# Kernel optimization log

Measured on AMD Instinct MI355X. Metric: run time of the kernel, lower is better.

Reference implementation:

```python
import jax, jax.numpy as jnp
from jax import lax
import numpy as np

H, W = 240, 304
IN_CH, OUT_CH, K = 16, 32, 3
B = 8
N_PER = 65536
N = B * N_PER
CIN = IN_CH + 2  # pos + neg + features


def setup_inputs() -> dict:
    key = jax.random.key(0)
    k1, k2, k3, k4, k5 = jax.random.split(key, 5)
    # events columns: x, y, t in [0,1); polarity in {0,1}
    xyt = jax.random.uniform(k1, (N, 3), dtype=jnp.float32)
    pol = jax.random.randint(k2, (N, 1), 0, 2).astype(jnp.float32)
    events = jnp.concatenate([xyt, pol], axis=1)
    features = jax.random.normal(k3, (N, IN_CH), dtype=jnp.float32)
    offsets = (jnp.arange(1, B + 1, dtype=jnp.int64) * N_PER)  # cumulative counts
    # SubmanifoldConvolution params: one [CIN, OUT_CH] matrix per filter offset -> HWIO
    fan_in = K * K * CIN
    weight = jax.random.normal(k4, (K, K, CIN, OUT_CH), dtype=jnp.float32) / np.sqrt(fan_in)
    bias = jax.random.normal(k5, (OUT_CH,), dtype=jnp.float32) * 0.01
    return {"events": events, "features": features, "weight": weight,
            "bias": bias, "offsets": offsets}


def reference(events, features, weight, bias, offsets):
    n = events.shape[0]
    b = offsets.shape[0]
    # offset2batch: row i belongs to first sample whose cumulative offset exceeds i
    batch = jnp.searchsorted(offsets, jnp.arange(n, dtype=offsets.dtype), side="right").astype(jnp.int32)
    pos = events[:, 3:4]
    neg = 1.0 - pos
    sparse = jnp.concatenate([pos, neg, features], axis=1)  # [N, CIN]
    # yx = events[:, [1, 0]] scaled by (h, w), rounded to grid coords
    yi = jnp.clip(jnp.round(events[:, 1] * H).astype(jnp.int32), 0, H - 1)
    xi = jnp.clip(jnp.round(events[:, 0] * W).astype(jnp.int32), 0, W - 1)
    key = (batch * H + yi) * W + xi  # linear site id, [N]
    nseg = b * H * W
    # scn InputLayer mode=4: average features of duplicate coordinates
    feat_sum = jax.ops.segment_sum(sparse, key, num_segments=nseg)  # [nseg, CIN]
    cnt = jax.ops.segment_sum(jnp.ones((n,), sparse.dtype), key, num_segments=nseg)
    dense = feat_sum / jnp.maximum(cnt, 1.0)[:, None]
    dense = dense.reshape(b, H, W, CIN)  # zeros at inactive sites
    # Submanifold 3x3 conv: inactive neighbors are zero, so a dense SAME conv
    # evaluated only at active sites matches the submanifold rulebook math.
    out = lax.conv_general_dilated(dense, weight, window_strides=(1, 1),
                                   padding="SAME",
                                   dimension_numbers=("NHWC", "HWIO", "NHWC"))
    out = out.reshape(nseg, OUT_CH)
    # OutputLayer: read back per input row (active sites only), add bias there
    f = out[key] + bias  # [N, OUT_CH]
    return f
```

## Files before the change

kernel.cpp:

```cpp
#include <hip/hip_runtime.h>

#define Hh 240
#define Ww 304
#define IN_CH 16
#define OUT_CH 32
#define Bb 8
#define N_PER 65536
#define N_EV (Bb * N_PER)
#define CIN (IN_CH + 2)
#define NSEG (Bb * Hh * Ww)
#define NBLK 570

#define TW 32
#define TH 8
#define HW_ 34
#define HH_ 10
#define NXT_TILES 10
#define NYT_TILES 30
#define OPITCH 33

typedef __attribute__((ext_vector_type(8))) short bf16x8;
typedef __attribute__((ext_vector_type(4))) float f32x4;

__device__ __forceinline__ unsigned short f2bf(float x) {
  unsigned u = __float_as_uint(x);
  unsigned r = u + 0x7fffu + ((u >> 16) & 1u);
  return (unsigned short)(r >> 16);
}
__device__ __forceinline__ float bf2f(unsigned short b) {
  return __uint_as_float(((unsigned)b) << 16);
}

__global__ __launch_bounds__(256) void hist_rank_kernel(
    const float* __restrict__ events, const int* __restrict__ offsets,
    int* __restrict__ hist, int* __restrict__ keyArr, int* __restrict__ rankArr) {
  int i = blockIdx.x * blockDim.x + threadIdx.x;
  float4 ev = ((const float4*)events)[i];
  int yi = (int)rintf(ev.y * (float)Hh);
  yi = min(max(yi, 0), Hh - 1);
  int xi = (int)rintf(ev.x * (float)Ww);
  xi = min(max(xi, 0), Ww - 1);
  int b = 0;
#pragma unroll
  for (int j = 0; j < Bb; j++) b += (offsets[j] <= i) ? 1 : 0;
  int key = (b * Hh + yi) * Ww + xi;
  int pol = (ev.w != 0.0f) ? 1 : 0;
  keyArr[i] = key | (pol << 31);
  rankArr[i] = atomicAdd(&hist[key], 1);
}

__global__ __launch_bounds__(256) void scan1_kernel(
    const int* __restrict__ hist, int* __restrict__ baseLocal,
    int* __restrict__ blockSum) {
  __shared__ int lds[256];
  int b = blockIdx.x, t = threadIdx.x;
  int idx = b * 1024 + t * 4;
  int4 v = *(const int4*)(hist + idx);
  int s0 = v.x, s1 = s0 + v.y, s2 = s1 + v.z, s3 = s2 + v.w;
  lds[t] = s3;
  __syncthreads();
  int val = s3;
  for (int off = 1; off < 256; off <<= 1) {
    int n = (t >= off) ? lds[t - off] : 0;
    __syncthreads();
    val += n;
    lds[t] = val;
    __syncthreads();
  }
  int excl = val - s3;
  int4 o;
  o.x = excl; o.y = excl + s0; o.z = excl + s1; o.w = excl + s2;
  *(int4*)(baseLocal + idx) = o;
  if (t == 255) blockSum[b] = val;
}

__global__ __launch_bounds__(1024) void scan2_kernel(
    const int* __restrict__ blockSum, int* __restrict__ blockOffset) {
  __shared__ int lds[1024];
  int t = threadIdx.x;
  int v = (t < NBLK) ? blockSum[t] : 0;
  lds[t] = v;
  __syncthreads();
  int val = v;
  for (int off = 1; off < 1024; off <<= 1) {
    int n = (t >= off) ? lds[t - off] : 0;
    __syncthreads();
    val += n;
    lds[t] = val;
    __syncthreads();
  }
  if (t < NBLK) blockOffset[t] = val - v;
  if (t == 0) blockOffset[NBLK] = lds[1023];
}

__global__ __launch_bounds__(256) void scatter_feat_kernel(
    const float* __restrict__ features, const int* __restrict__ keyArr,
    const int* __restrict__ rankArr, const int* __restrict__ baseLocal,
    const int* __restrict__ blockOffset, uint4* __restrict__ sortedFeat,
    int* __restrict__ sortedMeta) {
  int i = blockIdx.x * blockDim.x + threadIdx.x;
  int meta = keyArr[i];
  int key = meta & 0x7fffffff;
  int pos = baseLocal[key] + blockOffset[key >> 10] + rankArr[i];
  const float4* f = (const float4*)(features + (size_t)i * IN_CH);
  float4 f0 = f[0], f1 = f[1], f2 = f[2], f3 = f[3];
  uint4 w0, w1;
  w0.x = (unsigned)f2bf(f0.x) | ((unsigned)f2bf(f0.y) << 16);
  w0.y = (unsigned)f2bf(f0.z) | ((unsigned)f2bf(f0.w) << 16);
  w0.z = (unsigned)f2bf(f1.x) | ((unsigned)f2bf(f1.y) << 16);
  w0.w = (unsigned)f2bf(f1.z) | ((unsigned)f2bf(f1.w) << 16);
  w1.x = (unsigned)f2bf(f2.x) | ((unsigned)f2bf(f2.y) << 16);
  w1.y = (unsigned)f2bf(f2.z) | ((unsigned)f2bf(f2.w) << 16);
  w1.z = (unsigned)f2bf(f3.x) | ((unsigned)f2bf(f3.y) << 16);
  w1.w = (unsigned)f2bf(f3.z) | ((unsigned)f2bf(f3.w) << 16);
  sortedFeat[(size_t)pos * 2] = w0;
  sortedFeat[(size_t)pos * 2 + 1] = w1;
  sortedMeta[pos] = i | (meta & 0x80000000);
}

__global__ __launch_bounds__(256) void fused_conv_kernel(
    const uint4* __restrict__ sortedFeat, const int* __restrict__ sortedMeta,
    const int* __restrict__ baseLocal, const int* __restrict__ blockOffset,
    const float* __restrict__ weight, const float* __restrict__ bias,
    float* __restrict__ out) {
  __shared__ unsigned smem[256 * OPITCH];
  __shared__ int ibase[TH * TW];
  __shared__ int icnt[TH * TW];

  int blk = blockIdx.x;
  int xt = blk % NXT_TILES;
  int rem = blk / NXT_TILES;
  int yt = rem % NYT_TILES;
  int b = rem / NYT_TILES;
  int x0 = xt * TW, y0 = yt * TH;
  int tid = threadIdx.x;

  if (tid < 12) smem[3060 + tid] = 0;

  for (int h = tid; h < HH_ * HW_; h += 256) {
    int hy = h / HW_, hx = h % HW_;
    int gy = y0 - 1 + hy, gx = x0 - 1 + hx;
    float acc[CIN];
#pragma unroll
    for (int k = 0; k < CIN; k++) acc[k] = 0.0f;
    int c = 0, base = 0;
    if (gy >= 0 && gy < Hh && gx >= 0 && gx < Ww) {
      int p = (b * Hh + gy) * Ww + gx;
      int bo = blockOffset[p >> 10];
      base = baseLocal[p] + bo;
      int nxt = ((p & 1023) != 1023) ? (baseLocal[p + 1] + bo)
                                     : blockOffset[(p >> 10) + 1];
      c = nxt - base;
      for (int j = 0; j < c; j++) {
        int e = sortedMeta[base + j];
        float pol = (float)((unsigned)e >> 31);
        acc[0] += pol;
        acc[1] += 1.0f - pol;
        uint4 w0 = sortedFeat[(size_t)(base + j) * 2];
        uint4 w1 = sortedFeat[(size_t)(base + j) * 2 + 1];
        acc[2] += bf2f((unsigned short)w0.x);  acc[3] += bf2f((unsigned short)(w0.x >> 16));
        acc[4] += bf2f((unsigned short)w0.y);  acc[5] += bf2f((unsigned short)(w0.y >> 16));
        acc[6] += bf2f((unsigned short)w0.z);  acc[7] += bf2f((unsigned short)(w0.z >> 16));
        acc[8] += bf2f((unsigned short)w0.w);  acc[9] += bf2f((unsigned short)(w0.w >> 16));
        acc[10] += bf2f((unsigned short)w1.x); acc[11] += bf2f((unsigned short)(w1.x >> 16));
        acc[12] += bf2f((unsigned short)w1.y); acc[13] += bf2f((unsigned short)(w1.y >> 16));
        acc[14] += bf2f((unsigned short)w1.z); acc[15] += bf2f((unsigned short)(w1.z >> 16));
        acc[16] += bf2f((unsigned short)w1.w); acc[17] += bf2f((unsigned short)(w1.w >> 16));
      }
    }
    float inv = 1.0f / fmaxf((float)c, 1.0f);
    unsigned* row = smem + 9 * h;
#pragma unroll
    for (int k = 0; k < 9; k++)
      row[k] = (unsigned)f2bf(acc[2 * k] * inv) |
               ((unsigned)f2bf(acc[2 * k + 1] * inv) << 16);
    if (hx >= 1 && hx <= TW && hy >= 1 && hy <= TH) {
      int t = (hy - 1) * TW + (hx - 1);
      ibase[t] = base;
      icnt[t] = c;
    }
  }
  __syncthreads();

  int wv = tid >> 6, lane = tid & 63;
  int quad = lane >> 4, lrow = lane & 15;

  bf16x8 bfr[3][2][2];
#pragma unroll
  for (int ky = 0; ky < 3; ky++) {
#pragma unroll
    for (int kh = 0; kh < 2; kh++) {
#pragma unroll
      for (int nt = 0; nt < 2; nt++) {
        int n = nt * 16 + lrow;
#pragma unroll
        for (int j = 0; j < 8; j++) {
          int kl = kh * 32 + quad * 8 + j;
          short w = 0;
          if (kl < 54) {
            int kx = kl / 18, ci = kl - kx * 18;
            w = (short)f2bf(weight[((ky * 3 + kx) * CIN + ci) * OUT_CH + n]);
          }
          bfr[ky][kh][nt][j] = w;
        }
      }
    }
  }

  f32x4 accf[4][2];
#pragma unroll
  for (int i = 0; i < 4; i++)
#pragma unroll
    for (int nt = 0; nt < 2; nt++) accf[i][nt] = (f32x4){0.f, 0.f, 0.f, 0.f};

  const unsigned* hp = smem;
#pragma unroll
  for (int i = 0; i < 4; i++) {
    int t0 = (wv * 4 + i) * 16;
    int ox = (t0 & 31) + lrow;
    int oy = t0 >> 5;
#pragma unroll
    for (int ky = 0; ky < 3; ky++) {
      int idx0 = ((oy + ky) * HW_ + ox) * CIN;
#pragma unroll
      for (int kh = 0; kh < 2; kh++) {
        union { bf16x8 v; unsigned u[4]; } a;
        int ui = (idx0 >> 1) + kh * 16 + quad * 4;
        a.u[0] = hp[ui]; a.u[1] = hp[ui + 1];
        a.u[2] = hp[ui + 2]; a.u[3] = hp[ui + 3];
        accf[i][0] = __builtin_amdgcn_mfma_f32_16x16x32_bf16(
            a.v, bfr[ky][kh][0], accf[i][0], 0, 0, 0);
        accf[i][1] = __builtin_amdgcn_mfma_f32_16x16x32_bf16(
            a.v, bfr[ky][kh][1], accf[i][1], 0, 0, 0);
      }
    }
  }
  __syncthreads();

  float* outsh = (float*)smem;
  float bn0 = bias[lrow], bn1 = bias[16 + lrow];
#pragma unroll
  for (int i = 0; i < 4; i++) {
    int tb = (wv * 4 + i) * 16 + quad * 4;
#pragma unroll
    for (int r = 0; r < 4; r++) {
      outsh[(tb + r) * OPITCH + lrow] = accf[i][0][r] + bn0;
      outsh[(tb + r) * OPITCH + 16 + lrow] = accf[i][1][r] + bn1;
    }
  }
  __syncthreads();

  int gx = x0 + (tid & 31);
  int c = icnt[tid];
  int base = ibase[tid];
  if (gx < Ww && c > 0) {
    const float* row = outsh + tid * OPITCH;
    float4 o0 = make_float4(row[0], row[1], row[2], row[3]);
    float4 o1 = make_float4(row[4], row[5], row[6], row[7]);
    float4 o2 = make_float4(row[8], row[9], row[10], row[11]);
    float4 o3 = make_float4(row[12], row[13], row[14], row[15]);
    float4 o4 = make_float4(row[16], row[17], row[18], row[19]);
    float4 o5 = make_float4(row[20], row[21], row[22], row[23]);
    float4 o6 = make_float4(row[24], row[25], row[26], row[27]);
    float4 o7 = make_float4(row[28], row[29], row[30], row[31]);
    for (int j = 0; j < c; j++) {
      int ev = sortedMeta[base + j] & 0x7fffffff;
      float4* op = (float4*)(out + (size_t)ev * OUT_CH);
      op[0] = o0; op[1] = o1; op[2] = o2; op[3] = o3;
      op[4] = o4; op[5] = o5; op[6] = o6; op[7] = o7;
    }
  }
}

extern "C" void kernel_launch(void* const* d_in, const int* in_sizes, int n_in,
                              void* d_out, int out_size, void* d_ws,
                              size_t ws_size, hipStream_t stream) {
  const float* events = (const float*)d_in[0];
  const float* features = (const float*)d_in[1];
  const float* weight = (const float*)d_in[2];
  const float* bias = (const float*)d_in[3];
  const int* offsets = (const int*)d_in[4];
  float* out = (float*)d_out;

  uint4* sortedFeat = (uint4*)d_ws;
  int* sortedMeta = (int*)(sortedFeat + (size_t)N_EV * 2);
  int* keyArr = sortedMeta + N_EV;
  int* rankArr = keyArr + N_EV;
  int* hist = rankArr + N_EV;
  int* baseLocal = hist + NSEG;
  int* blockOffset = baseLocal + NSEG;
  int* blockSum = blockOffset + 1024;

  hipMemsetAsync(hist, 0, (size_t)NSEG * sizeof(int), stream);

  hist_rank_kernel<<<N_EV / 256, 256, 0, stream>>>(events, offsets, hist,
                                                   keyArr, rankArr);
  scan1_kernel<<<NBLK, 256, 0, stream>>>(hist, baseLocal, blockSum);
  scan2_kernel<<<1, 1024, 0, stream>>>(blockSum, blockOffset);
  scatter_feat_kernel<<<N_EV / 256, 256, 0, stream>>>(
      features, keyArr, rankArr, baseLocal, blockOffset, sortedFeat, sortedMeta);
  fused_conv_kernel<<<Bb * NYT_TILES * NXT_TILES, 256, 0, stream>>>(
      sortedFeat, sortedMeta, baseLocal, blockOffset, weight, bias, out);
}
```

Measured before the change: 208.1 us.

## Prepack bf16 weights, stream per-ky B fragments, halve conv LDS footprint

A new one-block kernel converts the fp32 weights once into a packed bf16 layout, so each conv block loads its B fragments with vector loads instead of 48 scalar loads and conversions per lane. The ky loop is now the outer loop, so only one ky's fragments are live at a time, which cuts register pressure. The output staging buffer is halved and the write-out runs in two chunks with extra barriers, shrinking shared memory to allow more resident blocks per CU. The cost is one extra kernel launch, additional synchronisation, and reloading the weight fragments from global memory for each ky.

```diff
diff --git a/kernel.cpp b/kernel.cpp
--- a/kernel.cpp
+++ b/kernel.cpp
@@ -91,6 +91,25 @@
   }
   if (t < NBLK) blockOffset[t] = val - v;
   if (t == 0) blockOffset[NBLK] = lds[1023];
+}
+
+__global__ __launch_bounds__(256) void prep_weights_kernel(
+    const float* __restrict__ weight, unsigned short* __restrict__ wprep) {
+  int tid = threadIdx.x;
+#pragma unroll
+  for (int it = 0; it < 24; it++) {
+    int idx = it * 256 + tid;
+    int ky = idx >> 11;
+    int rem = idx & 2047;
+    int n = rem >> 6;
+    int kl = rem & 63;
+    unsigned short v = 0;
+    if (kl < 54) {
+      int kx = kl / 18, ci = kl - kx * 18;
+      v = f2bf(weight[((ky * 3 + kx) * CIN + ci) * OUT_CH + n]);
+    }
+    wprep[idx] = v;
+  }
 }
 
 __global__ __launch_bounds__(256) void scatter_feat_kernel(
@@ -121,9 +140,9 @@
 __global__ __launch_bounds__(256) void fused_conv_kernel(
     const uint4* __restrict__ sortedFeat, const int* __restrict__ sortedMeta,
     const int* __restrict__ baseLocal, const int* __restrict__ blockOffset,
-    const float* __restrict__ weight, const float* __restrict__ bias,
+    const unsigned short* __restrict__ wprep, const float* __restrict__ bias,
     float* __restrict__ out) {
-  __shared__ unsigned smem[256 * OPITCH];
+  __shared__ unsigned smem[128 * OPITCH];
   __shared__ int ibase[TH * TW];
   __shared__ int icnt[TH * TW];
 
@@ -185,42 +204,29 @@
   int wv = tid >> 6, lane = tid & 63;
   int quad = lane >> 4, lrow = lane & 15;
 
-  bf16x8 bfr[3][2][2];
+  f32x4 accf[4][2];
+#pragma unroll
+  for (int i = 0; i < 4; i++)
+#pragma unroll
+    for (int nt = 0; nt < 2; nt++) accf[i][nt] = (f32x4){0.f, 0.f, 0.f, 0.f};
+
+  const unsigned* hp = smem;
 #pragma unroll
   for (int ky = 0; ky < 3; ky++) {
-#pragma unroll
-    for (int kh = 0; kh < 2; kh++) {
+    bf16x8 bfr[2][2];
+#pragma unroll
+    for (int kh = 0; kh < 2; kh++)
 #pragma unroll
       for (int nt = 0; nt < 2; nt++) {
         int n = nt * 16 + lrow;
-#pragma unroll
-        for (int j = 0; j < 8; j++) {
-          int kl = kh * 32 + quad * 8 + j;
-          short w = 0;
-          if (kl < 54) {
-            int kx = kl / 18, ci = kl - kx * 18;
-            w = (short)f2bf(weight[((ky * 3 + kx) * CIN + ci) * OUT_CH + n]);
-          }
-          bfr[ky][kh][nt][j] = w;
-        }
-      }
-    }
-  }
-
-  f32x4 accf[4][2];
-#pragma unroll
-  for (int i = 0; i < 4; i++)
-#pragma unroll
-    for (int nt = 0; nt < 2; nt++) accf[i][nt] = (f32x4){0.f, 0.f, 0.f, 0.f};
-
-  const unsigned* hp = smem;
-#pragma unroll
-  for (int i = 0; i < 4; i++) {
-    int t0 = (wv * 4 + i) * 16;
-    int ox = (t0 & 31) + lrow;
-    int oy = t0 >> 5;
-#pragma unroll
-    for (int ky = 0; ky < 3; ky++) {
+        bfr[kh][nt] = *(const bf16x8*)(wprep + ((ky * 32 + n) << 6) +
+                                       kh * 32 + quad * 8);
+      }
+#pragma unroll
+    for (int i = 0; i < 4; i++) {
+      int t0 = (wv * 4 + i) * 16;
+      int ox = (t0 & 31) + lrow;
+      int oy = t0 >> 5;
       int idx0 = ((oy + ky) * HW_ + ox) * CIN;
 #pragma unroll
       for (int kh = 0; kh < 2; kh++) {
@@ -229,9 +235,9 @@
         a.u[0] = hp[ui]; a.u[1] = hp[ui + 1];
         a.u[2] = hp[ui + 2]; a.u[3] = hp[ui + 3];
         accf[i][0] = __builtin_amdgcn_mfma_f32_16x16x32_bf16(
-            a.v, bfr[ky][kh][0], accf[i][0], 0, 0, 0);
+            a.v, bfr[kh][0], accf[i][0], 0, 0, 0);
         accf[i][1] = __builtin_amdgcn_mfma_f32_16x16x32_bf16(
-            a.v, bfr[ky][kh][1], accf[i][1], 0, 0, 0);
+            a.v, bfr[kh][1], accf[i][1], 0, 0, 0);
       }
     }
   }
@@ -239,36 +245,42 @@
 
   float* outsh = (float*)smem;
   float bn0 = bias[lrow], bn1 = bias[16 + lrow];
-#pragma unroll
-  for (int i = 0; i < 4; i++) {
-    int tb = (wv * 4 + i) * 16 + quad * 4;
-#pragma unroll
-    for (int r = 0; r < 4; r++) {
-      outsh[(tb + r) * OPITCH + lrow] = accf[i][0][r] + bn0;
-      outsh[(tb + r) * OPITCH + 16 + lrow] = accf[i][1][r] + bn1;
-    }
-  }
-  __syncthreads();
-
   int gx = x0 + (tid & 31);
   int c = icnt[tid];
   int base = ibase[tid];
-  if (gx < Ww && c > 0) {
-    const float* row = outsh + tid * OPITCH;
-    float4 o0 = make_float4(row[0], row[1], row[2], row[3]);
-    float4 o1 = make_float4(row[4], row[5], row[6], row[7]);
-    float4 o2 = make_float4(row[8], row[9], row[10], row[11]);
-    float4 o3 = make_float4(row[12], row[13], row[14], row[15]);
-    float4 o4 = make_float4(row[16], row[17], row[18], row[19]);
-    float4 o5 = make_float4(row[20], row[21], row[22], row[23]);
-    float4 o6 = make_float4(row[24], row[25], row[26], row[27]);
-    float4 o7 = make_float4(row[28], row[29], row[30], row[31]);
-    for (int j = 0; j < c; j++) {
-      int ev = sortedMeta[base + j] & 0x7fffffff;
-      float4* op = (float4*)(out + (size_t)ev * OUT_CH);
-      op[0] = o0; op[1] = o1; op[2] = o2; op[3] = o3;
-      op[4] = o4; op[5] = o5; op[6] = o6; op[7] = o7;
-    }
+#pragma unroll
+  for (int ch = 0; ch < 2; ch++) {
+#pragma unroll
+    for (int ii = 0; ii < 2; ii++) {
+      int i = ch * 2 + ii;
+      int lidx = ii * 16 + quad * 4;
+      int row = wv * 32 + lidx;
+#pragma unroll
+      for (int r = 0; r < 4; r++) {
+        outsh[(row + r) * OPITCH + lrow] = accf[i][0][r] + bn0;
+        outsh[(row + r) * OPITCH + 16 + lrow] = accf[i][1][r] + bn1;
+      }
+    }
+    __syncthreads();
+    if (((tid >> 5) & 1) == ch && gx < Ww && c > 0) {
+      int row = (tid >> 6) * 32 + ((tid & 63) - ch * 32);
+      const float* rp = outsh + row * OPITCH;
+      float4 o0 = make_float4(rp[0], rp[1], rp[2], rp[3]);
+      float4 o1 = make_float4(rp[4], rp[5], rp[6], rp[7]);
+      float4 o2 = make_float4(rp[8], rp[9], rp[10], rp[11]);
+      float4 o3 = make_float4(rp[12], rp[13], rp[14], rp[15]);
+      float4 o4 = make_float4(rp[16], rp[17], rp[18], rp[19]);
+      float4 o5 = make_float4(rp[20], rp[21], rp[22], rp[23]);
+      float4 o6 = make_float4(rp[24], rp[25], rp[26], rp[27]);
+      float4 o7 = make_float4(rp[28], rp[29], rp[30], rp[31]);
+      for (int j = 0; j < c; j++) {
+        int ev = sortedMeta[base + j] & 0x7fffffff;
+        float4* op = (float4*)(out + (size_t)ev * OUT_CH);
+        op[0] = o0; op[1] = o1; op[2] = o2; op[3] = o3;
+        op[4] = o4; op[5] = o5; op[6] = o6; op[7] = o7;
+      }
+    }
+    __syncthreads();
   }
 }
 
@@ -290,15 +302,17 @@
   int* baseLocal = hist + NSEG;
   int* blockOffset = baseLocal + NSEG;
   int* blockSum = blockOffset + 1024;
+  unsigned short* wprep = (unsigned short*)(blockSum + 1024);
 
   hipMemsetAsync(hist, 0, (size_t)NSEG * sizeof(int), stream);
 
   hist_rank_kernel<<<N_EV / 256, 256, 0, stream>>>(events, offsets, hist,
                                                    keyArr, rankArr);
+  prep_weights_kernel<<<1, 256, 0, stream>>>(weight, wprep);
   scan1_kernel<<<NBLK, 256, 0, stream>>>(hist, baseLocal, blockSum);
   scan2_kernel<<<1, 1024, 0, stream>>>(blockSum, blockOffset);
   scatter_feat_kernel<<<N_EV / 256, 256, 0, stream>>>(
       features, keyArr, rankArr, baseLocal, blockOffset, sortedFeat, sortedMeta);
   fused_conv_kernel<<<Bb * NYT_TILES * NXT_TILES, 256, 0, stream>>>(
-      sortedFeat, sortedMeta, baseLocal, blockOffset, weight, bias, out);
-}
+      sortedFeat, sortedMeta, baseLocal, blockOffset, wprep, bias, out);
+}
```

Result: faster. 190.2 us (-8.6%).
